# Kernel optimization log

Hardware: AMD Instinct MI355X
Metric: run time of the kernel (lower is better)

The kernel has to match this reference:

```python
import jax, jax.numpy as jnp
import numpy as np

EPS = 1e-5          # module's self.eps
CLAMP = 1e-8        # numerical floor for norms
MAX_EUCLID = 32.0   # rescale_to_max_euclid cap (best-effort reconstruction)


def _linner(u, v):
    # Lorentz inner product <u,v>_L = -u0*v0 + <u_s,v_s>, keepdims on last axis
    uv = jnp.sum(u * v, axis=-1, keepdims=True)
    return uv - 2.0 * u[..., :1] * v[..., :1]


def _centroid(x):
    # Lorentzian (weighted) centroid: mean then renormalize onto hyperboloid (k=1)
    avg = jnp.mean(x, axis=-2)
    denom = jnp.sqrt(jnp.clip(-_linner(avg, avg), CLAMP, None))
    return avg / denom


def _logmap(x, y):
    # log_x(y) on Lorentz model, k=1
    alpha = jnp.clip(-_linner(x, y), 1.0 + 1e-7, None)
    u = y - alpha * x
    unorm = jnp.sqrt(jnp.clip(_linner(u, u), CLAMP, None))
    return jnp.arccosh(alpha) * u / unorm


def _plus_origin(y):
    # y + o where o = (1, 0, ..., 0)
    return jnp.concatenate([y[..., :1] + 1.0, y[..., 1:]], axis=-1)


def _transp0back(y, v):
    # parallel transport T_{y->o}(v): v + <o,v>_L/(1 - <y,o>_L) * (y + o); <o,v>_L = -v0
    coef = -v[..., :1] / (1.0 + y[..., :1])
    return v + coef * _plus_origin(y)


def _transp0(y, v):
    # parallel transport T_{o->y}(v): v + <y,v>_L/(1 + y0) * (o + y)
    coef = _linner(y, v) / (1.0 + y[..., :1])
    return v + coef * _plus_origin(y)


def _expmap(x, u):
    # exp_x(u) on Lorentz model, k=1
    nu = jnp.sqrt(jnp.clip(_linner(u, u), CLAMP, None))
    return jnp.cosh(nu) * x + jnp.sinh(nu) * u / nu


def _rescale_to_max_euclid(x):
    n = jnp.sqrt(jnp.sum(x * x, axis=-1, keepdims=True))
    return x * jnp.minimum(1.0, MAX_EUCLID / jnp.maximum(n, CLAMP))


def setup_inputs() -> dict:
    key = jax.random.key(0)
    B, S, D = 64, 4096, 128
    raw = 0.5 * jax.random.normal(key, (B, S, D - 1), dtype=jnp.float32)
    time = jnp.sqrt(1.0 + jnp.sum(raw * raw, axis=-1, keepdims=True))
    x = jnp.concatenate([time, raw], axis=-1)  # points on the hyperboloid
    gamma = jnp.ones((D,), dtype=jnp.float32)
    beta = jnp.zeros((D,), dtype=jnp.float32).at[0].set(1.0)  # manifold origin
    return {"x": x, "gamma": gamma, "beta": beta}


def reference(x, gamma, beta):
    # Training-mode Lorentz batchnorm (3D input path)
    mean = _centroid(x)       # (B, D)
    mean = _centroid(mean)    # (D,)
    x_T = _logmap(mean, x)            # tangent vectors at mean, (B, S, D)
    x_T = _transp0back(mean, x_T)     # transport to tangent space at origin
    var = jnp.sqrt(jnp.var(x_T, axis=(0, 1)) + EPS)   # Frechet per-feature std, (D,)
    x_T = x_T * (gamma / (var + EPS))
    x_T = _rescale_to_max_euclid(x_T)
    x_T = _transp0(beta, x_T)         # transport to tangent space at beta
    return _expmap(beta, x_T)
```

## Files before the change

kernel.cpp:

```cpp
#include <hip/hip_runtime.h>
#include <math.h>

#define NB 64
#define NS 4096
#define ND 128
#define NPTS (NB * NS)
#define PPB1 128
#define NBLK1 (NPTS / PPB1)
#define CHUNKS1 (NS / PPB1)
#define PPB 128
#define NBLK (NPTS / PPB)
#define ITERS (PPB / 16)
#define EPSV 1e-5f
#define CLAMPV 1e-8f
#define MAXEUC 32.0f

typedef float nfloat4 __attribute__((ext_vector_type(4)));

__device__ __forceinline__ void nt_store4(const float4& v, float4* p) {
    nfloat4 nv = {v.x, v.y, v.z, v.w};
    __builtin_nontemporal_store(nv, (nfloat4*)p);
}

__device__ __forceinline__ float rcp_f(float x) { return __builtin_amdgcn_rcpf(x); }

#define DPP_ADD(v, ctrl)                                                            \
    v += __int_as_float(__builtin_amdgcn_update_dpp(0, __float_as_int(v), (ctrl),   \
                                                    0xF, 0xF, true))

__device__ __forceinline__ float row16_sum(float v) {
    DPP_ADD(v, 0x128);
    DPP_ADD(v, 0x124);
    DPP_ADD(v, 0x122);
    DPP_ADD(v, 0x121);
    return v;
}

__device__ __forceinline__ void point_scalars16(const float4& xa, const float4& xb,
                                                const float4& wa, const float4& wb,
                                                float inv1pm0, int fl,
                                                float& fac, float& hcoef) {
    float ad = wa.x * xa.x + wa.y * xa.y + wa.z * xa.z + wa.w * xa.w
             + wb.x * xb.x + wb.y * xb.y + wb.z * xb.z + wb.w * xb.w;
    float px = (fl == 0) ? xa.x : 0.f;
    ad = row16_sum(ad);
    px = row16_sum(px);
    float alpha = fmaxf(ad, 1.0f + 1e-7f);
    float am1 = alpha * alpha - 1.f;
    float sq = sqrtf(fmaxf(am1, CLAMPV));
    fac = __logf(alpha + sq) * rcp_f(sq);
    hcoef = -fac * (alpha + px) * inv1pm0;
}

__global__ __launch_bounds__(256, 8) void k1(const float4* __restrict__ x4,
                                             float4* __restrict__ part1_4) {
    const int tid = threadIdx.x;
    const long long base = (long long)blockIdx.x * (PPB1 * 32);
    float4 acc = make_float4(0.f, 0.f, 0.f, 0.f);
#pragma unroll 8
    for (int i = 0; i < PPB1 * 32 / 256; ++i) {
        float4 v = x4[base + i * 256 + tid];
        acc.x += v.x; acc.y += v.y; acc.z += v.z; acc.w += v.w;
    }
    __shared__ float4 ls4[8][32];
    ls4[tid >> 5][tid & 31] = acc;
    __syncthreads();
    if (tid < 32) {
        float4 s = ls4[0][tid];
#pragma unroll
        for (int c = 1; c < 8; ++c) {
            float4 v = ls4[c][tid];
            s.x += v.x; s.y += v.y; s.z += v.z; s.w += v.w;
        }
        part1_4[blockIdx.x * 32 + tid] = s;
    }
}

__global__ __launch_bounds__(1024) void k2(const float* __restrict__ part1,
                                           float* __restrict__ meanG) {
    __shared__ float avgL[NB][ND];
    const int w = threadIdx.x >> 6, l = threadIdx.x & 63;
    for (int b = w; b < NB; b += 16) {
        float a0 = 0.f, a1 = 0.f;
#pragma unroll
        for (int c = 0; c < CHUNKS1; ++c) {
            a0 += part1[(b * CHUNKS1 + c) * ND + l];
            a1 += part1[(b * CHUNKS1 + c) * ND + 64 + l];
        }
        a0 *= (1.0f / (float)NS);
        a1 *= (1.0f / (float)NS);
        float s = a0 * a0 + a1 * a1;
#pragma unroll
        for (int o = 32; o > 0; o >>= 1) s += __shfl_xor(s, o, 64);
        float a00 = __shfl(a0, 0, 64);
        float denom = sqrtf(fmaxf(2.f * a00 * a00 - s, CLAMPV));
        avgL[b][l] = a0 / denom;
        avgL[b][64 + l] = a1 / denom;
    }
    __syncthreads();
    if (w == 0) {
        float a0 = 0.f, a1 = 0.f;
        for (int b = 0; b < NB; ++b) { a0 += avgL[b][l]; a1 += avgL[b][64 + l]; }
        a0 *= (1.0f / (float)NB);
        a1 *= (1.0f / (float)NB);
        float s = a0 * a0 + a1 * a1;
#pragma unroll
        for (int o = 32; o > 0; o >>= 1) s += __shfl_xor(s, o, 64);
        float a00 = __shfl(a0, 0, 64);
        float denom = sqrtf(fmaxf(2.f * a00 * a00 - s, CLAMPV));
        meanG[l] = a0 / denom;
        meanG[64 + l] = a1 / denom;
    }
}

__global__ __launch_bounds__(256, 4) void k3(const float4* __restrict__ x4,
                                             const float* __restrict__ meanG,
                                             float* __restrict__ p3S,
                                             float* __restrict__ p3Q,
                                             float2* __restrict__ fchG) {
    const int fl = threadIdx.x & 15;
    const int pg = threadIdx.x >> 4;
    const float4* m4 = (const float4*)meanG;
    const float4 ma = m4[fl], mb = m4[fl + 16];
    const float m0 = meanG[0];
    const float inv1pm0 = rcp_f(1.f + m0);
    float4 wa = make_float4(-ma.x, -ma.y, -ma.z, -ma.w);
    float4 wb = make_float4(-mb.x, -mb.y, -mb.z, -mb.w);
    if (fl == 0) wa.x = ma.x;
    float4 sa = make_float4(0.f, 0.f, 0.f, 0.f), sb = sa, qa = sa, qb = sa;
    const long long base = (long long)blockIdx.x * PPB;
    float4 xa = x4[(base + pg) * 32 + fl];
    float4 xb = x4[(base + pg) * 32 + fl + 16];
#pragma unroll
    for (int i = 0; i < ITERS; ++i) {
        float4 na, nb;
        if (i + 1 < ITERS) {
            long long pn = base + (i + 1) * 16 + pg;
            na = x4[pn * 32 + fl];
            nb = x4[pn * 32 + fl + 16];
        }
        long long p = base + i * 16 + pg;
        float fac, hc;
        point_scalars16(xa, xb, wa, wb, inv1pm0, fl, fac, hc);
        if (fl == 0) fchG[p] = make_float2(fac, hc);
        float t0 = fac * xa.x + hc * ma.x;
        float t1 = fac * xa.y + hc * ma.y;
        float t2 = fac * xa.z + hc * ma.z;
        float t3 = fac * xa.w + hc * ma.w;
        float t4 = fac * xb.x + hc * mb.x;
        float t5 = fac * xb.y + hc * mb.y;
        float t6 = fac * xb.z + hc * mb.z;
        float t7 = fac * xb.w + hc * mb.w;
        if (fl == 0) t0 = 0.f;
        sa.x += t0; sa.y += t1; sa.z += t2; sa.w += t3;
        sb.x += t4; sb.y += t5; sb.z += t6; sb.w += t7;
        qa.x += t0 * t0; qa.y += t1 * t1; qa.z += t2 * t2; qa.w += t3 * t3;
        qb.x += t4 * t4; qb.y += t5 * t5; qb.z += t6 * t6; qb.w += t7 * t7;
        xa = na; xb = nb;
    }
    __shared__ float ls[16][ND];
    __shared__ float lq[16][ND];
    float* ps = &ls[pg][fl * 8];
    float* pq = &lq[pg][fl * 8];
    ps[0] = sa.x; ps[1] = sa.y; ps[2] = sa.z; ps[3] = sa.w;
    ps[4] = sb.x; ps[5] = sb.y; ps[6] = sb.z; ps[7] = sb.w;
    pq[0] = qa.x; pq[1] = qa.y; pq[2] = qa.z; pq[3] = qa.w;
    pq[4] = qb.x; pq[5] = qb.y; pq[6] = qb.z; pq[7] = qb.w;
    __syncthreads();
    if (threadIdx.x < ND) {
        int d = threadIdx.x;
        int slot = ((d & 63) >> 2) * 8 + (d >> 6) * 4 + (d & 3);
        float S = 0.f, Q = 0.f;
#pragma unroll
        for (int cc = 0; cc < 16; ++cc) { S += ls[cc][slot]; Q += lq[cc][slot]; }
        p3S[d * NBLK + blockIdx.x] = S;
        p3Q[d * NBLK + blockIdx.x] = Q;
    }
}

__global__ __launch_bounds__(256) void k4(const float* __restrict__ p3S,
                                          const float* __restrict__ p3Q,
                                          const float* __restrict__ gamma,
                                          float* __restrict__ scaleG) {
    const int d = blockIdx.x;
    const int t = threadIdx.x;
    const float4* vS = (const float4*)(p3S + d * NBLK);
    const float4* vQ = (const float4*)(p3Q + d * NBLK);
    float4 a0 = vS[t], a1 = vS[t + 256];
    float4 b0 = vQ[t], b1 = vQ[t + 256];
    __shared__ double dredS[256];
    __shared__ double dredQ[256];
    dredS[t] = (double)a0.x + (double)a0.y + (double)a0.z + (double)a0.w
             + (double)a1.x + (double)a1.y + (double)a1.z + (double)a1.w;
    dredQ[t] = (double)b0.x + (double)b0.y + (double)b0.z + (double)b0.w
             + (double)b1.x + (double)b1.y + (double)b1.z + (double)b1.w;
    __syncthreads();
    for (int o = 128; o > 0; o >>= 1) {
        if (t < o) { dredS[t] += dredS[t + o]; dredQ[t] += dredQ[t + o]; }
        __syncthreads();
    }
    if (t == 0) {
        const double N = (double)NPTS;
        double mu = dredS[0] / N;
        double var = dredQ[0] / N - mu * mu;
        if (var < 0.0) var = 0.0;
        float stdv = sqrtf((float)var + EPSV);
        scaleG[d] = gamma[d] / (stdv + EPSV);
    }
}

__global__ __launch_bounds__(256, 4) void k5(const float4* __restrict__ x4,
                                             const float* __restrict__ meanG,
                                             const float* __restrict__ scaleG,
                                             const float* __restrict__ betaG,
                                             const float2* __restrict__ fchG,
                                             float4* __restrict__ out4) {
    const int fl = threadIdx.x & 15;
    const int pg = threadIdx.x >> 4;
    const float4* m4 = (const float4*)meanG;
    const float4* s4 = (const float4*)scaleG;
    const float4* b4 = (const float4*)betaG;
    const float4 ma = m4[fl], mb = m4[fl + 16];
    const float4 sca = s4[fl], scb = s4[fl + 16];
    const float4 bta = b4[fl], btb = b4[fl + 16];
    const float b0 = betaG[0];
    const float inv1pb0 = rcp_f(1.f + b0);
    const long long base = (long long)blockIdx.x * PPB;
    float4 xa = x4[(base + pg) * 32 + fl];
    float4 xb = x4[(base + pg) * 32 + fl + 16];
    float2 fh = fchG[base + pg];
#pragma unroll
    for (int i = 0; i < ITERS; ++i) {
        float4 na, nb; float2 nf;
        if (i + 1 < ITERS) {
            long long pn = base + (i + 1) * 16 + pg;
            na = x4[pn * 32 + fl];
            nb = x4[pn * 32 + fl + 16];
            nf = fchG[pn];
        }
        long long p = base + i * 16 + pg;
        float fac = fh.x, hc = fh.y;
        float ts0 = sca.x * (fac * xa.x + hc * ma.x);
        float ts1 = sca.y * (fac * xa.y + hc * ma.y);
        float ts2 = sca.z * (fac * xa.z + hc * ma.z);
        float ts3 = sca.w * (fac * xa.w + hc * ma.w);
        float ts4 = scb.x * (fac * xb.x + hc * mb.x);
        float ts5 = scb.y * (fac * xb.y + hc * mb.y);
        float ts6 = scb.z * (fac * xb.z + hc * mb.z);
        float ts7 = scb.w * (fac * xb.w + hc * mb.w);
        if (fl == 0) ts0 = 0.f;
        float nn = ts0 * ts0 + ts1 * ts1 + ts2 * ts2 + ts3 * ts3
                 + ts4 * ts4 + ts5 * ts5 + ts6 * ts6 + ts7 * ts7;
        float bd = bta.x * ts0 + bta.y * ts1 + bta.z * ts2 + bta.w * ts3
                 + btb.x * ts4 + btb.y * ts5 + btb.z * ts6 + btb.w * ts7;
        nn = row16_sum(nn);
        bd = row16_sum(bd);
        float n = sqrtf(nn);
        float r = fminf(1.f, MAXEUC * rcp_f(fmaxf(n, CLAMPV)));
        float coef2 = r * bd * inv1pb0;
        float nu = fmaxf(r * n, 1e-4f);
        float e = __expf(nu);
        float ei = rcp_f(e);
        float ch = 0.5f * (e + ei);
        float sf = (0.5f * (e - ei)) * rcp_f(nu);
        float A = ch + sf * coef2;
        float Bc = sf * r;
        float4 oa, ob;
        oa.x = Bc * ts0 + A * bta.x;
        oa.y = Bc * ts1 + A * bta.y;
        oa.z = Bc * ts2 + A * bta.z;
        oa.w = Bc * ts3 + A * bta.w;
        ob.x = Bc * ts4 + A * btb.x;
        ob.y = Bc * ts5 + A * btb.y;
        ob.z = Bc * ts6 + A * btb.z;
        ob.w = Bc * ts7 + A * btb.w;
        if (fl == 0) oa.x += sf * coef2;
        nt_store4(oa, &out4[p * 32 + fl]);
        nt_store4(ob, &out4[p * 32 + fl + 16]);
        xa = na; xb = nb; fh = nf;
    }
}

extern "C" void kernel_launch(void* const* d_in, const int* in_sizes, int n_in,
                              void* d_out, int out_size, void* d_ws, size_t ws_size,
                              hipStream_t stream) {
    const float* x = (const float*)d_in[0];
    const float* gamma = (const float*)d_in[1];
    const float* beta = (const float*)d_in[2];
    float* out = (float*)d_out;
    float* ws = (float*)d_ws;

    float* part1  = ws;
    float* meanG  = part1 + NBLK1 * ND;
    float* scaleG = meanG + ND;
    float* p3S    = scaleG + ND;
    float* p3Q    = p3S + ND * NBLK;
    float2* fchG  = (float2*)(p3Q + ND * NBLK);

    k1<<<NBLK1, 256, 0, stream>>>((const float4*)x, (float4*)part1);
    k2<<<1, 1024, 0, stream>>>(part1, meanG);
    k3<<<NBLK, 256, 0, stream>>>((const float4*)x, meanG, p3S, p3Q, fchG);
    k4<<<ND, 256, 0, stream>>>(p3S, p3Q, gamma, scaleG);
    k5<<<NBLK, 256, 0, stream>>>((const float4*)x, meanG, scaleG, beta, fchG,
                                 (float4*)out);
}
```

Before: 295.1 us.

## Split centroid kernel across blocks, raise occupancy hints, use plain stores

Replaces the single-block k2 with two kernels: k2a computes per-batch centroids in 64 parallel blocks, and k2b reduces them to the global mean. This targets the serial latency of one 1024-thread block walking all batches, at the cost of one extra launch and an intermediate buffer in global memory. It also raises the min-blocks hint on k3 and k5 from 4 to 6, which may tighten register limits. It swaps the nontemporal output stores for ordinary stores.

```diff
diff --git a/kernel.cpp b/kernel.cpp
--- a/kernel.cpp
+++ b/kernel.cpp
@@ -14,13 +14,6 @@
 #define EPSV 1e-5f
 #define CLAMPV 1e-8f
 #define MAXEUC 32.0f
-
-typedef float nfloat4 __attribute__((ext_vector_type(4)));
-
-__device__ __forceinline__ void nt_store4(const float4& v, float4* p) {
-    nfloat4 nv = {v.x, v.y, v.z, v.w};
-    __builtin_nontemporal_store(nv, (nfloat4*)p);
-}
 
 __device__ __forceinline__ float rcp_f(float x) { return __builtin_amdgcn_rcpf(x); }
 
@@ -76,44 +69,47 @@
     }
 }
 
-__global__ __launch_bounds__(1024) void k2(const float* __restrict__ part1,
-                                           float* __restrict__ meanG) {
-    __shared__ float avgL[NB][ND];
-    const int w = threadIdx.x >> 6, l = threadIdx.x & 63;
-    for (int b = w; b < NB; b += 16) {
-        float a0 = 0.f, a1 = 0.f;
-#pragma unroll
-        for (int c = 0; c < CHUNKS1; ++c) {
-            a0 += part1[(b * CHUNKS1 + c) * ND + l];
-            a1 += part1[(b * CHUNKS1 + c) * ND + 64 + l];
-        }
-        a0 *= (1.0f / (float)NS);
-        a1 *= (1.0f / (float)NS);
-        float s = a0 * a0 + a1 * a1;
-#pragma unroll
-        for (int o = 32; o > 0; o >>= 1) s += __shfl_xor(s, o, 64);
-        float a00 = __shfl(a0, 0, 64);
-        float denom = sqrtf(fmaxf(2.f * a00 * a00 - s, CLAMPV));
-        avgL[b][l] = a0 / denom;
-        avgL[b][64 + l] = a1 / denom;
-    }
-    __syncthreads();
-    if (w == 0) {
-        float a0 = 0.f, a1 = 0.f;
-        for (int b = 0; b < NB; ++b) { a0 += avgL[b][l]; a1 += avgL[b][64 + l]; }
-        a0 *= (1.0f / (float)NB);
-        a1 *= (1.0f / (float)NB);
-        float s = a0 * a0 + a1 * a1;
-#pragma unroll
-        for (int o = 32; o > 0; o >>= 1) s += __shfl_xor(s, o, 64);
-        float a00 = __shfl(a0, 0, 64);
-        float denom = sqrtf(fmaxf(2.f * a00 * a00 - s, CLAMPV));
-        meanG[l] = a0 / denom;
-        meanG[64 + l] = a1 / denom;
-    }
-}
-
-__global__ __launch_bounds__(256, 4) void k3(const float4* __restrict__ x4,
+__global__ __launch_bounds__(64) void k2a(const float* __restrict__ part1,
+                                          float* __restrict__ avg1) {
+    const int b = blockIdx.x;
+    const int t = threadIdx.x;
+    float a0 = 0.f, a1 = 0.f;
+#pragma unroll
+    for (int c = 0; c < CHUNKS1; ++c) {
+        a0 += part1[(b * CHUNKS1 + c) * ND + t];
+        a1 += part1[(b * CHUNKS1 + c) * ND + 64 + t];
+    }
+    a0 *= (1.0f / (float)NS);
+    a1 *= (1.0f / (float)NS);
+    float s = a0 * a0 + a1 * a1;
+#pragma unroll
+    for (int o = 32; o > 0; o >>= 1) s += __shfl_xor(s, o, 64);
+    float a00 = __shfl(a0, 0, 64);
+    float denom = sqrtf(fmaxf(2.f * a00 * a00 - s, CLAMPV));
+    avg1[b * ND + t] = a0 / denom;
+    avg1[b * ND + 64 + t] = a1 / denom;
+}
+
+__global__ __launch_bounds__(64) void k2b(const float* __restrict__ avg1,
+                                          float* __restrict__ meanG) {
+    const int t = threadIdx.x;
+    float a0 = 0.f, a1 = 0.f;
+    for (int b = 0; b < NB; ++b) {
+        a0 += avg1[b * ND + t];
+        a1 += avg1[b * ND + 64 + t];
+    }
+    a0 *= (1.0f / (float)NB);
+    a1 *= (1.0f / (float)NB);
+    float s = a0 * a0 + a1 * a1;
+#pragma unroll
+    for (int o = 32; o > 0; o >>= 1) s += __shfl_xor(s, o, 64);
+    float a00 = __shfl(a0, 0, 64);
+    float denom = sqrtf(fmaxf(2.f * a00 * a00 - s, CLAMPV));
+    meanG[t] = a0 / denom;
+    meanG[64 + t] = a1 / denom;
+}
+
+__global__ __launch_bounds__(256, 6) void k3(const float4* __restrict__ x4,
                                              const float* __restrict__ meanG,
                                              float* __restrict__ p3S,
                                              float* __restrict__ p3Q,
@@ -209,7 +205,7 @@
     }
 }
 
-__global__ __launch_bounds__(256, 4) void k5(const float4* __restrict__ x4,
+__global__ __launch_bounds__(256, 6) void k5(const float4* __restrict__ x4,
                                              const float* __restrict__ meanG,
                                              const float* __restrict__ scaleG,
                                              const float* __restrict__ betaG,
@@ -275,8 +271,8 @@
         ob.z = Bc * ts6 + A * btb.z;
         ob.w = Bc * ts7 + A * btb.w;
         if (fl == 0) oa.x += sf * coef2;
-        nt_store4(oa, &out4[p * 32 + fl]);
-        nt_store4(ob, &out4[p * 32 + fl + 16]);
+        out4[p * 32 + fl] = oa;
+        out4[p * 32 + fl + 16] = ob;
         xa = na; xb = nb; fh = nf;
     }
 }
@@ -291,16 +287,18 @@
     float* ws = (float*)d_ws;
 
     float* part1  = ws;
-    float* meanG  = part1 + NBLK1 * ND;
+    float* avg1   = part1 + NBLK1 * ND;
+    float* meanG  = avg1 + NB * ND;
     float* scaleG = meanG + ND;
     float* p3S    = scaleG + ND;
     float* p3Q    = p3S + ND * NBLK;
     float2* fchG  = (float2*)(p3Q + ND * NBLK);
 
-    k1<<<NBLK1, 256, 0, stream>>>((const float4*)x, (float4*)part1);
-    k2<<<1, 1024, 0, stream>>>(part1, meanG);
-    k3<<<NBLK, 256, 0, stream>>>((const float4*)x, meanG, p3S, p3Q, fchG);
-    k4<<<ND, 256, 0, stream>>>(p3S, p3Q, gamma, scaleG);
-    k5<<<NBLK, 256, 0, stream>>>((const float4*)x, meanG, scaleG, beta, fchG,
-                                 (float4*)out);
-}
+    k1 <<<NBLK1, 256, 0, stream>>>((const float4*)x, (float4*)part1);
+    k2a<<<NB, 64, 0, stream>>>(part1, avg1);
+    k2b<<<1, 64, 0, stream>>>(avg1, meanG);
+    k3 <<<NBLK, 256, 0, stream>>>((const float4*)x, meanG, p3S, p3Q, fchG);
+    k4 <<<ND, 256, 0, stream>>>(p3S, p3Q, gamma, scaleG);
+    k5 <<<NBLK, 256, 0, stream>>>((const float4*)x, meanG, scaleG, beta, fchG,
+                                  (float4*)out);
+}
```

After: 356.4 us. 20.8% more time.
